# Performance work log

Measured on AMD Instinct MI355X. Metric: run time of the kernel, lower is better.

The kernel has to match this reference:

```python
import jax, jax.numpy as jnp
import numpy as np

NUM_LEVELS = 16
LEVEL_DIM = 2
BASE_RES = 16
MAX_RES = 2048
LOG2_T = 21
TABLE_SIZE = 1 << LOG2_T
HASH_MASK = TABLE_SIZE - 1
BBOX_SCALE = 2.0
N_POINTS = 262144

# per-level integer resolutions, exactly as int(np.floor(base * b**i))
_b = np.exp((np.log(MAX_RES) - np.log(BASE_RES)) / (NUM_LEVELS - 1))
RESOLUTIONS = np.array([int(np.floor(BASE_RES * _b ** i)) for i in range(NUM_LEVELS)], dtype=np.float32)

PRIMES = np.array([73856093, 19349663, 83492791], dtype=np.int32)
# 8 corner offsets of the unit cube, same order as the torch module
OFFSETS = np.array([[0, 0, 0], [0, 0, 1], [0, 1, 0], [0, 1, 1],
                    [1, 0, 0], [1, 0, 1], [1, 1, 0], [1, 1, 1]], dtype=np.int32)


def setup_inputs() -> dict:
    key = jax.random.key(0)
    kx, kt = jax.random.split(key)
    x = jax.random.normal(kx, (N_POINTS, 3), dtype=jnp.float32)
    # nn.init.uniform_(w, a=-1e-4, b=1e-4) for each level, stacked
    tables = jax.random.uniform(kt, (NUM_LEVELS, TABLE_SIZE, LEVEL_DIM),
                                dtype=jnp.float32, minval=-1e-4, maxval=1e-4)
    return {"x": x, "tables": tables}


def reference(x, tables):
    # x: [N,3]; tables: [L,T,D]
    res = jnp.asarray(RESOLUTIONS)                      # [L]
    primes = jnp.asarray(PRIMES)                        # [3]
    offsets = jnp.asarray(OFFSETS)                      # [8,3]

    x_norm = jnp.clip((x + BBOX_SCALE) / (2 * BBOX_SCALE), 0.0, 1.0)   # [N,3]
    scaled = x_norm[None, :, :] * res[:, None, None]    # [L,N,3]
    x0 = jnp.floor(scaled).astype(jnp.int32)            # [L,N,3] (non-negative)
    w = scaled - x0.astype(jnp.float32)                 # [L,N,3] trilinear fractions

    # all 8 corners at once: [L,N,8,3]
    corners = x0[:, :, None, :] + offsets[None, None, :, :]
    # spatial hash: xor of coord*prime; low 21 bits are identical whether
    # computed in int64 (torch) or wrapping int32, since we mask to 2^21.
    cp = corners * primes                                # [L,N,8,3] int32 (wraps)
    idx = (cp[..., 0] ^ cp[..., 1] ^ cp[..., 2]) & HASH_MASK   # [L,N,8]

    # per-level gather: [L,N,8,D]
    emb = jax.vmap(lambda t, i: t[i])(tables, idx)

    # trilinear weights: prod_k (offset_k ? w_k : 1-w_k) -> [L,N,8]
    wc = jnp.where(offsets[None, None, :, :] == 0,
                   1.0 - w[:, :, None, :], w[:, :, None, :]).prod(axis=-1)

    feat = jnp.einsum('lnc,lncd->lnd', wc, emb)          # [L,N,D]
    # torch.cat(features, dim=-1): level-major along last dim
    out = jnp.transpose(feat, (1, 0, 2)).reshape(x.shape[0], NUM_LEVELS * LEVEL_DIM)
    return out
```

## Files before the change

kernel.cpp:

```cpp
#include <hip/hip_runtime.h>
#include <math.h>

#define NUM_LEVELS 16
#define LOG2_T 21
#define TABLE_SIZE (1u << LOG2_T)
#define HASH_MASK (TABLE_SIZE - 1u)
#define N_POINTS 262144
#define GRID_P1 1024
#define PTS_PER_BLOCK 2048
#define PX 73856093u
#define PY 19349663u
#define PZ 83492791u

struct Args { float r[NUM_LEVELS]; int l2nc[NUM_LEVELS]; };

__global__ __launch_bounds__(256) void hash_embed_phase1_v9(
    const float* __restrict__ x,
    const float* __restrict__ tables,
    float2* __restrict__ wsbuf,
    Args args)
{
    const int bid = blockIdx.x;
    const int slot = bid & 7;
    const int slice = bid >> 3;
    const int base = slice * PTS_PER_BLOCK + threadIdx.x;

    #pragma unroll 1
    for (int li = 0; li < 2; ++li) {
        const int lv = (li == 0) ? slot : 15 - slot;
        const float r = args.r[lv];
        const int l2nc = args.l2nc[lv];
        const int shift = LOG2_T - l2nc;
        const int nc = 1 << l2nc;
        const float* __restrict__ tab =
            tables + (size_t)lv * ((size_t)TABLE_SIZE * 2);

        uint32_t hx[8], hy[8], hz[8];
        float wxx[8], wyy[8], wzz[8], a0[8], a1[8];
        #pragma unroll
        for (int p = 0; p < 8; ++p) {
            const int n = base + p * 256;
            const float px = x[n * 3 + 0];
            const float py = x[n * 3 + 1];
            const float pz = x[n * 3 + 2];
            const float nx = fminf(fmaxf((px + 2.0f) * 0.25f, 0.0f), 1.0f);
            const float ny = fminf(fmaxf((py + 2.0f) * 0.25f, 0.0f), 1.0f);
            const float nz = fminf(fmaxf((pz + 2.0f) * 0.25f, 0.0f), 1.0f);
            const float sx = nx * r, sy = ny * r, sz = nz * r;
            const float fx = floorf(sx), fy = floorf(sy), fz = floorf(sz);
            wxx[p] = sx - fx; wyy[p] = sy - fy; wzz[p] = sz - fz;
            hx[p] = (uint32_t)(int)fx * PX;
            hy[p] = (uint32_t)(int)fy * PY;
            hz[p] = (uint32_t)(int)fz * PZ;
            a0[p] = 0.0f; a1[p] = 0.0f;
        }

        #pragma unroll 1
        for (int c = 0; c < nc; ++c) {
            const uint32_t dummy_off = ((uint32_t)c << shift) << 3;
            #pragma unroll
            for (int p = 0; p < 8; ++p) {
                const uint32_t X0 = hx[p], Y0 = hy[p], Z0 = hz[p];
                const uint32_t X1 = X0 + PX, Y1 = Y0 + PY, Z1 = Z0 + PZ;
                const float qx = wxx[p], qy = wyy[p], qz = wzz[p];
                const float ax = 1.0f - qx, ay = 1.0f - qy, az = 1.0f - qz;

                uint32_t off[8]; float wc[8];
                #pragma unroll
                for (int i = 0; i < 8; ++i) {
                    const uint32_t h = ((i & 4) ? X1 : X0) ^ ((i & 2) ? Y1 : Y0)
                                     ^ ((i & 1) ? Z1 : Z0);
                    const uint32_t idx = h & HASH_MASK;
                    const bool m = (idx >> shift) == (uint32_t)c;
                    off[i] = m ? (idx << 3) : dummy_off;
                    wc[i]  = m ? ((((i & 4) ? qx : ax) * ((i & 2) ? qy : ay))
                                  * ((i & 1) ? qz : az))
                               : 0.0f;
                }
                float2 t0, t1, t2, t3, t4, t5, t6, t7;
                asm volatile("global_load_dwordx2 %0, %1, %2" : "=v"(t0) : "v"(off[0]), "s"(tab));
                asm volatile("global_load_dwordx2 %0, %1, %2" : "=v"(t1) : "v"(off[1]), "s"(tab));
                asm volatile("global_load_dwordx2 %0, %1, %2" : "=v"(t2) : "v"(off[2]), "s"(tab));
                asm volatile("global_load_dwordx2 %0, %1, %2" : "=v"(t3) : "v"(off[3]), "s"(tab));
                asm volatile("global_load_dwordx2 %0, %1, %2" : "=v"(t4) : "v"(off[4]), "s"(tab));
                asm volatile("global_load_dwordx2 %0, %1, %2" : "=v"(t5) : "v"(off[5]), "s"(tab));
                asm volatile("global_load_dwordx2 %0, %1, %2" : "=v"(t6) : "v"(off[6]), "s"(tab));
                asm volatile("global_load_dwordx2 %0, %1, %2" : "=v"(t7) : "v"(off[7]), "s"(tab));
                asm volatile("s_waitcnt vmcnt(0)"
                             : "+v"(t0), "+v"(t1), "+v"(t2), "+v"(t3),
                               "+v"(t4), "+v"(t5), "+v"(t6), "+v"(t7));
                a0[p] = fmaf(wc[0], t0.x, a0[p]); a1[p] = fmaf(wc[0], t0.y, a1[p]);
                a0[p] = fmaf(wc[1], t1.x, a0[p]); a1[p] = fmaf(wc[1], t1.y, a1[p]);
                a0[p] = fmaf(wc[2], t2.x, a0[p]); a1[p] = fmaf(wc[2], t2.y, a1[p]);
                a0[p] = fmaf(wc[3], t3.x, a0[p]); a1[p] = fmaf(wc[3], t3.y, a1[p]);
                a0[p] = fmaf(wc[4], t4.x, a0[p]); a1[p] = fmaf(wc[4], t4.y, a1[p]);
                a0[p] = fmaf(wc[5], t5.x, a0[p]); a1[p] = fmaf(wc[5], t5.y, a1[p]);
                a0[p] = fmaf(wc[6], t6.x, a0[p]); a1[p] = fmaf(wc[6], t6.y, a1[p]);
                a0[p] = fmaf(wc[7], t7.x, a0[p]); a1[p] = fmaf(wc[7], t7.y, a1[p]);
            }
        }

        #pragma unroll
        for (int p = 0; p < 8; ++p) {
            wsbuf[(size_t)lv * N_POINTS + base + p * 256] = make_float2(a0[p], a1[p]);
        }
    }
}

__global__ __launch_bounds__(256) void hash_embed_phase2(
    const float2* __restrict__ ws,
    float2* __restrict__ out)
{
    __shared__ float2 tile[64][NUM_LEVELS + 1];
    const int n0 = blockIdx.x * 64;
    const int t = threadIdx.x;
    #pragma unroll
    for (int k = 0; k < 4; ++k) {
        const int e = k * 256 + t;
        const int l = e >> 6;
        const int j = e & 63;
        tile[j][l] = ws[(size_t)l * N_POINTS + n0 + j];
    }
    __syncthreads();
    #pragma unroll
    for (int k = 0; k < 4; ++k) {
        const int e = k * 256 + t;
        const int nl = e >> 4;
        const int l = e & 15;
        out[(size_t)(n0 + nl) * NUM_LEVELS + l] = tile[nl][l];
    }
}

__global__ __launch_bounds__(256) void hash_embed_direct(
    const float* __restrict__ x,
    const float* __restrict__ tables,
    float* __restrict__ out,
    Args args)
{
    const int t = blockIdx.x * blockDim.x + threadIdx.x;
    const int n = t >> 4;
    const int l = t & 15;
    if (n >= N_POINTS) return;

    const float px = x[n * 3 + 0];
    const float py = x[n * 3 + 1];
    const float pz = x[n * 3 + 2];
    const float nx = fminf(fmaxf((px + 2.0f) * 0.25f, 0.0f), 1.0f);
    const float ny = fminf(fmaxf((py + 2.0f) * 0.25f, 0.0f), 1.0f);
    const float nz = fminf(fmaxf((pz + 2.0f) * 0.25f, 0.0f), 1.0f);

    const float r = args.r[l];
    const float sx = nx * r, sy = ny * r, sz = nz * r;
    const float fx = floorf(sx), fy = floorf(sy), fz = floorf(sz);
    const float wxv = sx - fx, wyv = sy - fy, wzv = sz - fz;

    const uint32_t hx0 = (uint32_t)(int)fx * PX;
    const uint32_t hy0 = (uint32_t)(int)fy * PY;
    const uint32_t hz0 = (uint32_t)(int)fz * PZ;
    const uint32_t hx1 = hx0 + PX, hy1 = hy0 + PY, hz1 = hz0 + PZ;

    const float ax = 1.0f - wxv, ay = 1.0f - wyv, az = 1.0f - wzv;
    const float* __restrict__ tab = tables + (size_t)l * ((size_t)TABLE_SIZE * 2);

    float f0 = 0.0f, f1 = 0.0f;
    #pragma unroll
    for (int c = 0; c < 8; ++c) {
        const uint32_t hh = ((c & 4) ? hx1 : hx0) ^ ((c & 2) ? hy1 : hy0)
                          ^ ((c & 1) ? hz1 : hz0);
        const uint32_t idx = hh & HASH_MASK;
        const float2 emb = *reinterpret_cast<const float2*>(tab + (size_t)idx * 2);
        const float w = (((c & 4) ? wxv : ax) * ((c & 2) ? wyv : ay)) * ((c & 1) ? wzv : az);
        f0 = fmaf(w, emb.x, f0);
        f1 = fmaf(w, emb.y, f1);
    }
    float2* o = reinterpret_cast<float2*>(out + (size_t)n * (NUM_LEVELS * 2) + l * 2);
    *o = make_float2(f0, f1);
}

extern "C" void kernel_launch(void* const* d_in, const int* in_sizes, int n_in,
                              void* d_out, int out_size, void* d_ws, size_t ws_size,
                              hipStream_t stream) {
    const float* x      = (const float*)d_in[0];
    const float* tables = (const float*)d_in[1];
    float* out          = (float*)d_out;

    Args args;
    const double b = exp((log(2048.0) - log(16.0)) / 15.0);
    for (int i = 0; i < NUM_LEVELS; ++i) {
        const double ri = floor(16.0 * pow(b, (double)i));
        args.r[i] = (float)ri;
        double E = (ri + 1.0) * (ri + 1.0) * (ri + 1.0);
        if (E > 1.8e6) E = 1.8e6;
        const double lines = 262144.0 * (1.0 - exp(-8.0 * E / 2097152.0));
        const double bytes = lines * 64.0;
        int nc = (int)ceil(bytes / 2.5e6);
        if (nc < 1) nc = 1;
        int l2 = 0;
        while ((1 << l2) < nc) ++l2;
        if (l2 > 3) l2 = 3;
        args.l2nc[i] = l2;
    }

    const size_t ws_needed = (size_t)NUM_LEVELS * N_POINTS * sizeof(float2);
    if (ws_size >= ws_needed) {
        float2* wsbuf = (float2*)d_ws;
        hipLaunchKernelGGL(hash_embed_phase1_v9, dim3(GRID_P1), dim3(256),
                           0, stream, x, tables, wsbuf, args);
        hipLaunchKernelGGL(hash_embed_phase2, dim3(N_POINTS / 64), dim3(256),
                           0, stream, wsbuf, (float2*)out);
    } else {
        const int total = N_POINTS * NUM_LEVELS;
        hipLaunchKernelGGL(hash_embed_direct, dim3((total + 255) / 256), dim3(256),
                           0, stream, x, tables, out, args);
    }
}
```

Before: 271.9 us.

## Compact per-chunk gathers into LDS queues instead of masked dummy loads

For hashed levels the old kernel issued all 8 corner loads per point per table chunk, redirecting non-matching corners to a dummy address. The new kernel compacts only the matching corners into a shared-memory queue using wave ballots and an atomic counter. It then gathers them and accumulates into shared-memory accumulators with LDS atomics, and entries past the queue capacity fall back to direct loads. Coarse levels skip chunking and use plain loads, and the chunk count becomes either 1 or 8. This aims to cut wasted gather traffic, but it adds LDS atomics, extra barriers and ballot overhead, and may lower occupancy because of about 36KB of shared memory.

```diff
diff --git a/kernel.cpp b/kernel.cpp
--- a/kernel.cpp
+++ b/kernel.cpp
@@ -8,26 +8,44 @@
 #define N_POINTS 262144
 #define GRID_P1 1024
 #define PTS_PER_BLOCK 2048
+#define CAP 2560
 #define PX 73856093u
 #define PY 19349663u
 #define PZ 83492791u
 
 struct Args { float r[NUM_LEVELS]; int l2nc[NUM_LEVELS]; };
 
-__global__ __launch_bounds__(256) void hash_embed_phase1_v9(
+__global__ __launch_bounds__(256) void hash_embed_phase1_v14(
     const float* __restrict__ x,
     const float* __restrict__ tables,
     float2* __restrict__ wsbuf,
     Args args)
 {
+    __shared__ uint32_t qmeta[CAP];
+    __shared__ float    qw[CAP];
+    __shared__ float    acc[PTS_PER_BLOCK*2];
+    __shared__ int      cnt;
+
+    const int tid = threadIdx.x;
     const int bid = blockIdx.x;
     const int slot = bid & 7;
     const int slice = bid >> 3;
-    const int base = slice * PTS_PER_BLOCK + threadIdx.x;
+    const int base = slice * PTS_PER_BLOCK + tid;
+    const int lane = tid & 63;
+    float2* accv = (float2*)acc;
+
+    float nxx[8], nyy[8], nzz[8];
+    #pragma unroll
+    for (int p = 0; p < 8; ++p) {
+        const int n = base + p * 256;
+        nxx[p] = fminf(fmaxf((x[n*3+0] + 2.0f) * 0.25f, 0.0f), 1.0f);
+        nyy[p] = fminf(fmaxf((x[n*3+1] + 2.0f) * 0.25f, 0.0f), 1.0f);
+        nzz[p] = fminf(fmaxf((x[n*3+2] + 2.0f) * 0.25f, 0.0f), 1.0f);
+    }
 
     #pragma unroll 1
     for (int li = 0; li < 2; ++li) {
-        const int lv = (li == 0) ? slot : 15 - slot;
+        const int lv = li ? (15 - slot) : slot;
         const float r = args.r[lv];
         const int l2nc = args.l2nc[lv];
         const int shift = LOG2_T - l2nc;
@@ -36,73 +54,98 @@
             tables + (size_t)lv * ((size_t)TABLE_SIZE * 2);
 
         uint32_t hx[8], hy[8], hz[8];
-        float wxx[8], wyy[8], wzz[8], a0[8], a1[8];
+        float qx[8], qy[8], qz[8];
         #pragma unroll
         for (int p = 0; p < 8; ++p) {
-            const int n = base + p * 256;
-            const float px = x[n * 3 + 0];
-            const float py = x[n * 3 + 1];
-            const float pz = x[n * 3 + 2];
-            const float nx = fminf(fmaxf((px + 2.0f) * 0.25f, 0.0f), 1.0f);
-            const float ny = fminf(fmaxf((py + 2.0f) * 0.25f, 0.0f), 1.0f);
-            const float nz = fminf(fmaxf((pz + 2.0f) * 0.25f, 0.0f), 1.0f);
-            const float sx = nx * r, sy = ny * r, sz = nz * r;
+            const float sx = nxx[p]*r, sy = nyy[p]*r, sz = nzz[p]*r;
             const float fx = floorf(sx), fy = floorf(sy), fz = floorf(sz);
-            wxx[p] = sx - fx; wyy[p] = sy - fy; wzz[p] = sz - fz;
+            qx[p] = sx - fx; qy[p] = sy - fy; qz[p] = sz - fz;
             hx[p] = (uint32_t)(int)fx * PX;
             hy[p] = (uint32_t)(int)fy * PY;
             hz[p] = (uint32_t)(int)fz * PZ;
-            a0[p] = 0.0f; a1[p] = 0.0f;
         }
 
-        #pragma unroll 1
-        for (int c = 0; c < nc; ++c) {
-            const uint32_t dummy_off = ((uint32_t)c << shift) << 3;
+        if (l2nc == 0) {
             #pragma unroll
             for (int p = 0; p < 8; ++p) {
                 const uint32_t X0 = hx[p], Y0 = hy[p], Z0 = hz[p];
                 const uint32_t X1 = X0 + PX, Y1 = Y0 + PY, Z1 = Z0 + PZ;
-                const float qx = wxx[p], qy = wyy[p], qz = wzz[p];
-                const float ax = 1.0f - qx, ay = 1.0f - qy, az = 1.0f - qz;
-
-                uint32_t off[8]; float wc[8];
+                const float vqx = qx[p], vqy = qy[p], vqz = qz[p];
+                const float ax = 1.0f - vqx, ay = 1.0f - vqy, az = 1.0f - vqz;
+                float a0 = 0.0f, a1 = 0.0f;
                 #pragma unroll
                 for (int i = 0; i < 8; ++i) {
-                    const uint32_t h = ((i & 4) ? X1 : X0) ^ ((i & 2) ? Y1 : Y0)
-                                     ^ ((i & 1) ? Z1 : Z0);
-                    const uint32_t idx = h & HASH_MASK;
-                    const bool m = (idx >> shift) == (uint32_t)c;
-                    off[i] = m ? (idx << 3) : dummy_off;
-                    wc[i]  = m ? ((((i & 4) ? qx : ax) * ((i & 2) ? qy : ay))
-                                  * ((i & 1) ? qz : az))
-                               : 0.0f;
+                    const uint32_t idx = (((i&4)?X1:X0) ^ ((i&2)?Y1:Y0)
+                                        ^ ((i&1)?Z1:Z0)) & HASH_MASK;
+                    const float2 e = *(const float2*)(tab + (size_t)idx * 2);
+                    const float w = (((i&4)?vqx:ax) * ((i&2)?vqy:ay)) * ((i&1)?vqz:az);
+                    a0 = fmaf(w, e.x, a0);
+                    a1 = fmaf(w, e.y, a1);
                 }
-                float2 t0, t1, t2, t3, t4, t5, t6, t7;
-                asm volatile("global_load_dwordx2 %0, %1, %2" : "=v"(t0) : "v"(off[0]), "s"(tab));
-                asm volatile("global_load_dwordx2 %0, %1, %2" : "=v"(t1) : "v"(off[1]), "s"(tab));
-                asm volatile("global_load_dwordx2 %0, %1, %2" : "=v"(t2) : "v"(off[2]), "s"(tab));
-                asm volatile("global_load_dwordx2 %0, %1, %2" : "=v"(t3) : "v"(off[3]), "s"(tab));
-                asm volatile("global_load_dwordx2 %0, %1, %2" : "=v"(t4) : "v"(off[4]), "s"(tab));
-                asm volatile("global_load_dwordx2 %0, %1, %2" : "=v"(t5) : "v"(off[5]), "s"(tab));
-                asm volatile("global_load_dwordx2 %0, %1, %2" : "=v"(t6) : "v"(off[6]), "s"(tab));
-                asm volatile("global_load_dwordx2 %0, %1, %2" : "=v"(t7) : "v"(off[7]), "s"(tab));
-                asm volatile("s_waitcnt vmcnt(0)"
-                             : "+v"(t0), "+v"(t1), "+v"(t2), "+v"(t3),
-                               "+v"(t4), "+v"(t5), "+v"(t6), "+v"(t7));
-                a0[p] = fmaf(wc[0], t0.x, a0[p]); a1[p] = fmaf(wc[0], t0.y, a1[p]);
-                a0[p] = fmaf(wc[1], t1.x, a0[p]); a1[p] = fmaf(wc[1], t1.y, a1[p]);
-                a0[p] = fmaf(wc[2], t2.x, a0[p]); a1[p] = fmaf(wc[2], t2.y, a1[p]);
-                a0[p] = fmaf(wc[3], t3.x, a0[p]); a1[p] = fmaf(wc[3], t3.y, a1[p]);
-                a0[p] = fmaf(wc[4], t4.x, a0[p]); a1[p] = fmaf(wc[4], t4.y, a1[p]);
-                a0[p] = fmaf(wc[5], t5.x, a0[p]); a1[p] = fmaf(wc[5], t5.y, a1[p]);
-                a0[p] = fmaf(wc[6], t6.x, a0[p]); a1[p] = fmaf(wc[6], t6.y, a1[p]);
-                a0[p] = fmaf(wc[7], t7.x, a0[p]); a1[p] = fmaf(wc[7], t7.y, a1[p]);
+                wsbuf[(size_t)lv*N_POINTS + base + p*256] = make_float2(a0, a1);
             }
-        }
-
-        #pragma unroll
-        for (int p = 0; p < 8; ++p) {
-            wsbuf[(size_t)lv * N_POINTS + base + p * 256] = make_float2(a0[p], a1[p]);
+        } else {
+            for (int e = tid; e < PTS_PER_BLOCK; e += 256)
+                accv[e] = make_float2(0.0f, 0.0f);
+
+            #pragma unroll 1
+            for (int c = 0; c < nc; ++c) {
+                if (tid == 0) cnt = 0;
+                __syncthreads();
+
+                #pragma unroll
+                for (int p = 0; p < 8; ++p) {
+                    const uint32_t X0 = hx[p], Y0 = hy[p], Z0 = hz[p];
+                    const uint32_t X1 = X0 + PX, Y1 = Y0 + PY, Z1 = Z0 + PZ;
+                    const float vqx = qx[p], vqy = qy[p], vqz = qz[p];
+                    const float ax = 1.0f - vqx, ay = 1.0f - vqy, az = 1.0f - vqz;
+                    const uint32_t ptid = (uint32_t)(tid + p*256);
+                    #pragma unroll
+                    for (int i = 0; i < 8; ++i) {
+                        const uint32_t idx = (((i&4)?X1:X0) ^ ((i&2)?Y1:Y0)
+                                            ^ ((i&1)?Z1:Z0)) & HASH_MASK;
+                        const bool m = (idx >> shift) == (uint32_t)c;
+                        const unsigned long long mk = __ballot(m);
+                        int bw = 0;
+                        if (lane == 0 && mk) bw = atomicAdd(&cnt, (int)__popcll(mk));
+                        bw = __shfl(bw, 0);
+                        if (m) {
+                            const int off = bw +
+                                (int)__popcll(mk & ((1ull << lane) - 1ull));
+                            const float w = (((i&4)?vqx:ax) * ((i&2)?vqy:ay))
+                                          * ((i&1)?vqz:az);
+                            if (off < CAP) {
+                                qmeta[off] = idx | (ptid << 21);
+                                qw[off] = w;
+                            } else {
+                                const float2 e = *(const float2*)(tab + (size_t)idx*2);
+                                atomicAdd(&acc[2*ptid],   w * e.x);
+                                atomicAdd(&acc[2*ptid+1], w * e.y);
+                            }
+                        }
+                    }
+                }
+                __syncthreads();
+
+                const int K = min(cnt, CAP);
+                for (int e = tid; e < K; e += 256) {
+                    const uint32_t mt = qmeta[e];
+                    const float w = qw[e];
+                    const uint32_t idx = mt & HASH_MASK;
+                    const int pt = (int)(mt >> 21);
+                    const float2 em = *(const float2*)(tab + (size_t)idx * 2);
+                    atomicAdd(&acc[2*pt],   w * em.x);
+                    atomicAdd(&acc[2*pt+1], w * em.y);
+                }
+                __syncthreads();
+            }
+
+            #pragma unroll
+            for (int p = 0; p < 8; ++p) {
+                const int ptid = tid + p*256;
+                wsbuf[(size_t)lv*N_POINTS + base + p*256] = accv[ptid];
+            }
+            __syncthreads();
         }
     }
 }
@@ -193,18 +236,13 @@
         if (E > 1.8e6) E = 1.8e6;
         const double lines = 262144.0 * (1.0 - exp(-8.0 * E / 2097152.0));
         const double bytes = lines * 64.0;
-        int nc = (int)ceil(bytes / 2.5e6);
-        if (nc < 1) nc = 1;
-        int l2 = 0;
-        while ((1 << l2) < nc) ++l2;
-        if (l2 > 3) l2 = 3;
-        args.l2nc[i] = l2;
+        args.l2nc[i] = (bytes <= 2.5e6) ? 0 : 3;
     }
 
     const size_t ws_needed = (size_t)NUM_LEVELS * N_POINTS * sizeof(float2);
     if (ws_size >= ws_needed) {
         float2* wsbuf = (float2*)d_ws;
-        hipLaunchKernelGGL(hash_embed_phase1_v9, dim3(GRID_P1), dim3(256),
+        hipLaunchKernelGGL(hash_embed_phase1_v14, dim3(GRID_P1), dim3(256),
                            0, stream, x, tables, wsbuf, args);
         hipLaunchKernelGGL(hash_embed_phase2, dim3(N_POINTS / 64), dim3(256),
                            0, stream, wsbuf, (float2*)out);
```

Measured after the change: 1.070 ms. +293.6%, slower.
